# Kernel tuning notes

Measured on AMD Instinct MI355X. Metric: run time of the kernel, lower is better.

## Reference

```python
import jax, jax.numpy as jnp
import numpy as np

B, C, H, W = 2, 256, 64, 64
HEADS = 4
K = 64  # max attendable keys per query
GROUPS = 32
EPS = 1e-6


def group_norm(x, scale, bias):
    b, c, h, w = x.shape
    xg = x.reshape(b, GROUPS, c // GROUPS, h, w)
    mean = xg.mean(axis=(2, 3, 4), keepdims=True)
    var = xg.var(axis=(2, 3, 4), keepdims=True)
    xn = ((xg - mean) * jax.lax.rsqrt(var + EPS)).reshape(b, c, h, w)
    return xn * scale[None, :, None, None] + bias[None, :, None, None]


def conv1x1(x, w, b):
    return jnp.einsum('oc,bchw->bohw', w, x) + b[None, :, None, None]


def setup_inputs() -> dict:
    key = jax.random.key(0)
    ks = jax.random.split(key, 8)
    x = jax.random.normal(ks[0], (B, C, H, W), dtype=jnp.float32)
    valid_indices_mask = jax.random.randint(ks[1], (H * W, K), 0, 2, dtype=jnp.int32)
    attendable_indices = jax.random.randint(ks[2], (H * W, K), 0, H * W, dtype=jnp.int32)
    s = 0.02
    wq = jax.random.normal(ks[3], (C, C), dtype=jnp.float32) * s
    wk = jax.random.normal(ks[4], (C, C), dtype=jnp.float32) * s
    wv = jax.random.normal(ks[5], (C, C), dtype=jnp.float32) * s
    wo = jax.random.normal(ks[6], (C, C), dtype=jnp.float32) * s
    return {
        'x': x,
        'valid_indices_mask': valid_indices_mask,
        'attendable_indices': attendable_indices,
        'gn_scale': jnp.ones((C,), jnp.float32),
        'gn_bias': jnp.zeros((C,), jnp.float32),
        'wq': wq, 'bq': jnp.zeros((C,), jnp.float32),
        'wk': wk, 'bk': jnp.zeros((C,), jnp.float32),
        'wv': wv, 'bv': jnp.zeros((C,), jnp.float32),
        'wo': wo, 'bo': jnp.zeros((C,), jnp.float32),
    }


def reference(x, valid_indices_mask, attendable_indices, gn_scale, gn_bias,
              wq, bq, wk, bk, wv, bv, wo, bo):
    b, c, h, w = x.shape
    nq = h * w
    d = c // HEADS
    h_ = group_norm(x, gn_scale, gn_bias)
    q = conv1x1(h_, wq, bq).reshape(b, HEADS, d, nq)
    k = conv1x1(h_, wk, bk).reshape(b, HEADS, d, nq)
    v = conv1x1(h_, wv, bv).reshape(b, HEADS, d, nq)
    # gather per-query attendable keys/values: [b, heads, nq, K, d]
    kt = k.transpose(0, 1, 3, 2)  # [b, heads, nv, d]
    vt = v.transpose(0, 1, 3, 2)
    ak = kt[:, :, attendable_indices]  # [b, heads, nq, K, d]
    av = vt[:, :, attendable_indices]
    # beta = 1 (no 1/sqrt(d) scaling in the sparse path, per original code)
    logits = jnp.einsum('bhqkc,bhcq->bhqk', ak, q)
    neg = jnp.where(valid_indices_mask == 0, -jnp.inf, 0.0).astype(logits.dtype)
    logits = logits + neg[None, None, :, :]
    weights = jax.nn.softmax(logits, axis=-1)
    attn = jnp.einsum('bhqk,bhqkc->bhqc', weights, av)  # [b, heads, nq, d]
    attn = attn.transpose(0, 3, 1, 2).reshape(b, c, h, w)
    out = x + conv1x1(attn, wo, bo)
    return out
```

## Files before the change

kernel.cpp:

```cpp
#include <hip/hip_runtime.h>
#include <math.h>

typedef unsigned int uint;
typedef unsigned short ushort;
typedef __attribute__((ext_vector_type(8))) short bf16x8;
typedef __attribute__((ext_vector_type(4))) float f32x4;

#define LSTR 40

__device__ __forceinline__ float bf2f(ushort u) { return __uint_as_float(((uint)u) << 16); }
__device__ __forceinline__ ushort f2bf(float f) {
    uint u = __float_as_uint(f);
    return (ushort)((u + 0x7fffu + ((u >> 16) & 1u)) >> 16);
}

__global__ __launch_bounds__(256) void gn_part_k(const float* __restrict__ x,
                                                 float* __restrict__ stats) {
    const int bg = blockIdx.x >> 2, part = blockIdx.x & 3;
    const float4* base = (const float4*)(x + (size_t)bg * 32768 + part * 8192);
    float s = 0.f, ss = 0.f;
    for (int i = threadIdx.x; i < 2048; i += 256) {
        float4 v = base[i];
        s  += v.x + v.y + v.z + v.w;
        ss += v.x*v.x + v.y*v.y + v.z*v.z + v.w*v.w;
    }
    #pragma unroll
    for (int o = 32; o; o >>= 1) { s += __shfl_xor(s, o); ss += __shfl_xor(ss, o); }
    if ((threadIdx.x & 63) == 0) {
        atomicAdd(&stats[bg * 2],     s);
        atomicAdd(&stats[bg * 2 + 1], ss);
    }
}

__global__ __launch_bounds__(256) void gn_apply_t_k(const float* __restrict__ x,
        const float* __restrict__ stats, const float* __restrict__ sc,
        const float* __restrict__ bi, ushort* __restrict__ hT) {
    const int n0 = blockIdx.x * 64, c0 = blockIdx.y * 64, b = blockIdx.z;
    __shared__ ushort tile[64][65];
    const int t = threadIdx.x;
    #pragma unroll
    for (int it = 0; it < 4; ++it) {
        const int r = (t >> 4) + it * 16, col4 = t & 15;
        const int c = c0 + r, bg = b * 32 + (c >> 3);
        const float S = stats[bg * 2], SS = stats[bg * 2 + 1];
        const float mean = S * (1.f / 32768.f);
        const float var  = SS * (1.f / 32768.f) - mean * mean;
        const float a  = rsqrtf(var + 1e-6f) * sc[c];
        const float bb = bi[c] - mean * a;
        float4 v = *(const float4*)(x + ((size_t)(b * 256 + c)) * 4096 + n0 + col4 * 4);
        tile[r][col4*4 + 0] = f2bf(v.x * a + bb);
        tile[r][col4*4 + 1] = f2bf(v.y * a + bb);
        tile[r][col4*4 + 2] = f2bf(v.z * a + bb);
        tile[r][col4*4 + 3] = f2bf(v.w * a + bb);
    }
    __syncthreads();
    #pragma unroll
    for (int it = 0; it < 2; ++it) {
        const int nr = (t >> 3) + it * 32, c8 = t & 7;
        uint4 st;
        ushort e0 = tile[c8*8+0][nr], e1 = tile[c8*8+1][nr];
        ushort e2 = tile[c8*8+2][nr], e3 = tile[c8*8+3][nr];
        ushort e4 = tile[c8*8+4][nr], e5 = tile[c8*8+5][nr];
        ushort e6 = tile[c8*8+6][nr], e7 = tile[c8*8+7][nr];
        st.x = (uint)e0 | ((uint)e1 << 16);
        st.y = (uint)e2 | ((uint)e3 << 16);
        st.z = (uint)e4 | ((uint)e5 << 16);
        st.w = (uint)e6 | ((uint)e7 << 16);
        *(uint4*)(hT + ((size_t)b * 4096 + n0 + nr) * 256 + c0 + c8 * 8) = st;
    }
}

__global__ __launch_bounds__(256) void wprep_k(
        const float* __restrict__ wq, const float* __restrict__ wk,
        const float* __restrict__ wv, const float* __restrict__ wo,
        const float* __restrict__ bq, const float* __restrict__ bk,
        const float* __restrict__ bv,
        ushort* __restrict__ wqkv, ushort* __restrict__ wo_p,
        float* __restrict__ bqkv) {
    const int i = blockIdx.x * 256 + threadIdx.x;
    if (i < 196608) {
        const int o = i >> 8, k = i & 255;
        const float* W = (o < 256) ? wq : ((o < 512) ? wk : wv);
        wqkv[i] = f2bf(W[(o & 255) * 256 + k]);
    } else if (i < 262144) {
        const int j = i - 196608;
        const int o = j >> 8, kp = j & 255;
        const int h = kp >> 6, d = kp & 63;
        wo_p[j] = f2bf(wo[o * 256 + d * 4 + h]);
    } else if (i < 262912) {
        const int o = i - 262144;
        bqkv[o] = (o < 256) ? bq[o] : ((o < 512) ? bk[o - 256] : bv[o - 512]);
    }
}

__global__ __launch_bounds__(256) void qkv_gemm_k(
        const ushort* __restrict__ Wqkv, const float* __restrict__ bqkv,
        const ushort* __restrict__ hT, ushort* __restrict__ qkvb) {
    const int nt = blockIdx.x, mt = blockIdx.y, b = blockIdx.z;
    __shared__ ushort As[128 * LSTR];
    __shared__ ushort Bs[128 * LSTR];
    const int t = threadIdx.x;
    const int wave = t >> 6, ln = t & 63;
    const int wm = wave >> 1, wn = wave & 1;
    f32x4 acc[4][4] = {};
    const ushort* Ag = Wqkv + (size_t)(mt * 128) * 256;
    const ushort* Bg = hT + ((size_t)b * 4096 + nt * 128) * 256;
    const int srow = t >> 2, sc8 = (t & 3) * 8;
    const int fr = ln & 15, kA = (ln >> 4) * 8;

    for (int k0 = 0; k0 < 256; k0 += 32) {
        #pragma unroll
        for (int i = 0; i < 2; ++i) {
            const int row = srow + i * 64;
            *(uint4*)&As[row * LSTR + sc8] = *(const uint4*)&Ag[(size_t)row * 256 + k0 + sc8];
            *(uint4*)&Bs[row * LSTR + sc8] = *(const uint4*)&Bg[(size_t)row * 256 + k0 + sc8];
        }
        __syncthreads();
        bf16x8 af[4], bfr[4];
        #pragma unroll
        for (int m = 0; m < 4; ++m) af[m]  = *(bf16x8*)&As[(wm * 64 + m * 16 + fr) * LSTR + kA];
        #pragma unroll
        for (int n = 0; n < 4; ++n) bfr[n] = *(bf16x8*)&Bs[(wn * 64 + n * 16 + fr) * LSTR + kA];
        #pragma unroll
        for (int m = 0; m < 4; ++m)
            #pragma unroll
            for (int n = 0; n < 4; ++n)
                acc[m][n] = __builtin_amdgcn_mfma_f32_16x16x32_bf16(af[m], bfr[n], acc[m][n], 0, 0, 0);
        __syncthreads();
    }
    const int colb = nt * 128 + wn * 64 + fr;
    const int rowb = mt * 128 + wm * 64;
    #pragma unroll
    for (int m = 0; m < 4; ++m) {
        const int o0 = rowb + m * 16 + ((ln >> 4) << 2);
        const int proj = o0 >> 8;
        const int head = (o0 >> 6) & 3;
        const int d0 = o0 & 63;
        const float4 bi4 = *(const float4*)&bqkv[o0];
        ushort* obase = qkvb + ((size_t)proj * 8 + (b * 4 + head)) * (4096 * 64) + d0;
        #pragma unroll
        for (int n = 0; n < 4; ++n) {
            const int nn = colb + n * 16;
            f32x4 a = acc[m][n];
            uint2 st;
            st.x = (uint)f2bf(a[0] + bi4.x) | ((uint)f2bf(a[1] + bi4.y) << 16);
            st.y = (uint)f2bf(a[2] + bi4.z) | ((uint)f2bf(a[3] + bi4.w) << 16);
            *(uint2*)&obase[(size_t)nn * 64] = st;
        }
    }
}

__global__ __launch_bounds__(256) void attn_k(
        const ushort* __restrict__ qb, const ushort* __restrict__ kb,
        const ushort* __restrict__ vb, const int* __restrict__ aidx,
        const int* __restrict__ vmask, ushort* __restrict__ attnb) {
    const int bh = blockIdx.x & 7;
    const int q4 = blockIdx.x >> 3;
    const int wave = threadIdx.x >> 6, ln = threadIdx.x & 63;
    const int n = q4 * 4 + wave;
    const ushort* kbase = kb + (size_t)bh * (4096 * 64);
    const ushort* vbase = vb + (size_t)bh * (4096 * 64);
    __shared__ float q_lds[4][64];
    q_lds[wave][ln] = bf2f(qb[(size_t)bh * (4096 * 64) + (size_t)n * 64 + ln]);
    const int idx = aidx[n * 64 + ln];
    const int msk = vmask[n * 64 + ln];
    __syncthreads();

    float dot = 0.f;
    if (msk) {
        const uint4* krow = (const uint4*)(kbase + (size_t)idx * 64);
        const float* qv = q_lds[wave];
        #pragma unroll
        for (int c = 0; c < 8; ++c) {
            uint4 u = krow[c];
            dot += __uint_as_float(u.x << 16)         * qv[c*8+0];
            dot += __uint_as_float(u.x & 0xffff0000u) * qv[c*8+1];
            dot += __uint_as_float(u.y << 16)         * qv[c*8+2];
            dot += __uint_as_float(u.y & 0xffff0000u) * qv[c*8+3];
            dot += __uint_as_float(u.z << 16)         * qv[c*8+4];
            dot += __uint_as_float(u.z & 0xffff0000u) * qv[c*8+5];
            dot += __uint_as_float(u.w << 16)         * qv[c*8+6];
            dot += __uint_as_float(u.w & 0xffff0000u) * qv[c*8+7];
        }
    }
    float mx = msk ? dot : -1e30f;
    #pragma unroll
    for (int o = 32; o; o >>= 1) mx = fmaxf(mx, __shfl_xor(mx, o));
    float e = msk ? __expf(dot - mx) : 0.f;
    float s = e;
    #pragma unroll
    for (int o = 32; o; o >>= 1) s += __shfl_xor(s, o);
    const float wgt = e / s;

    float a0 = 0.f, a1 = 0.f, a2 = 0.f, a3 = 0.f;
    #pragma unroll
    for (int kk = 0; kk < 64; kk += 4) {
        const float w0 = __shfl(wgt, kk),     w1 = __shfl(wgt, kk + 1);
        const float w2 = __shfl(wgt, kk + 2), w3 = __shfl(wgt, kk + 3);
        const int i0 = __shfl(idx, kk),     i1 = __shfl(idx, kk + 1);
        const int i2 = __shfl(idx, kk + 2), i3 = __shfl(idx, kk + 3);
        a0 += w0 * bf2f(vbase[(size_t)i0 * 64 + ln]);
        a1 += w1 * bf2f(vbase[(size_t)i1 * 64 + ln]);
        a2 += w2 * bf2f(vbase[(size_t)i2 * 64 + ln]);
        a3 += w3 * bf2f(vbase[(size_t)i3 * 64 + ln]);
    }
    const int b = bh >> 2, h = bh & 3;
    attnb[((size_t)b * 4096 + n) * 256 + h * 64 + ln] = f2bf(a0 + a1 + a2 + a3);
}

__global__ __launch_bounds__(256) void out_gemm_k(
        const ushort* __restrict__ wo_p, const float* __restrict__ bo,
        const ushort* __restrict__ attnb, const float* __restrict__ x,
        float* __restrict__ outp) {
    const int nt = blockIdx.x, mt = blockIdx.y, b = blockIdx.z;
    __shared__ ushort As[128 * LSTR];
    __shared__ ushort Bs[128 * LSTR];
    const int t = threadIdx.x;
    const int wave = t >> 6, ln = t & 63;
    const int wm = wave >> 1, wn = wave & 1;
    f32x4 acc[4][4] = {};
    const ushort* Ag = wo_p + (size_t)(mt * 128) * 256;
    const ushort* Bg = attnb + ((size_t)b * 4096 + nt * 128) * 256;
    const int srow = t >> 2, sc8 = (t & 3) * 8;
    const int fr = ln & 15, kA = (ln >> 4) * 8;

    for (int k0 = 0; k0 < 256; k0 += 32) {
        #pragma unroll
        for (int i = 0; i < 2; ++i) {
            const int row = srow + i * 64;
            *(uint4*)&As[row * LSTR + sc8] = *(const uint4*)&Ag[(size_t)row * 256 + k0 + sc8];
            *(uint4*)&Bs[row * LSTR + sc8] = *(const uint4*)&Bg[(size_t)row * 256 + k0 + sc8];
        }
        __syncthreads();
        bf16x8 af[4], bfr[4];
        #pragma unroll
        for (int m = 0; m < 4; ++m) af[m]  = *(bf16x8*)&As[(wm * 64 + m * 16 + fr) * LSTR + kA];
        #pragma unroll
        for (int n = 0; n < 4; ++n) bfr[n] = *(bf16x8*)&Bs[(wn * 64 + n * 16 + fr) * LSTR + kA];
        #pragma unroll
        for (int m = 0; m < 4; ++m)
            #pragma unroll
            for (int n = 0; n < 4; ++n)
                acc[m][n] = __builtin_amdgcn_mfma_f32_16x16x32_bf16(af[m], bfr[n], acc[m][n], 0, 0, 0);
        __syncthreads();
    }
    const int colb = nt * 128 + wn * 64 + fr;
    const int rowb = mt * 128 + wm * 64;
    #pragma unroll
    for (int m = 0; m < 4; ++m) {
        const int o0 = rowb + m * 16 + ((ln >> 4) << 2);
        const float4 bi4 = *(const float4*)&bo[o0];
        const float* bip = (const float*)&bi4;
        #pragma unroll
        for (int n = 0; n < 4; ++n) {
            const int nn = colb + n * 16;
            #pragma unroll
            for (int r = 0; r < 4; ++r) {
                const size_t a = ((size_t)(b * 256 + o0 + r)) * 4096 + nn;
                outp[a] = acc[m][n][r] + bip[r] + x[a];
            }
        }
    }
}

extern "C" void kernel_launch(void* const* d_in, const int* in_sizes, int n_in,
                              void* d_out, int out_size, void* d_ws, size_t ws_size,
                              hipStream_t stream) {
    const float* x     = (const float*)d_in[0];
    const int*   vmask = (const int*)d_in[1];
    const int*   aidx  = (const int*)d_in[2];
    const float* gsc   = (const float*)d_in[3];
    const float* gbi   = (const float*)d_in[4];
    const float* wq    = (const float*)d_in[5];
    const float* bq    = (const float*)d_in[6];
    const float* wk    = (const float*)d_in[7];
    const float* bk    = (const float*)d_in[8];
    const float* wv    = (const float*)d_in[9];
    const float* bv    = (const float*)d_in[10];
    const float* wo    = (const float*)d_in[11];
    const float* bo    = (const float*)d_in[12];
    float* outp = (float*)d_out;

    char* w = (char*)d_ws;
    float*  stats = (float*)w;
    ushort* wqkv  = (ushort*)(w + 1024);
    ushort* wo_p  = (ushort*)(w + 1024 + 393216);
    float*  bqkv  = (float*)(w + 525312);
    ushort* hT    = (ushort*)(w + 528384);
    ushort* qkvb  = (ushort*)(w + 4722688);
    ushort* attnb = (ushort*)(w + 17305600);

    ushort* qbuf = qkvb;
    ushort* kbuf = qkvb + 2097152;
    ushort* vbuf = qkvb + 4194304;

    hipMemsetAsync(stats, 0, 512, stream);
    hipLaunchKernelGGL(gn_part_k,    dim3(256),        dim3(256), 0, stream, x, stats);
    hipLaunchKernelGGL(wprep_k,      dim3(1027),       dim3(256), 0, stream,
                       wq, wk, wv, wo, bq, bk, bv, wqkv, wo_p, bqkv);
    hipLaunchKernelGGL(gn_apply_t_k, dim3(64, 4, 2),   dim3(256), 0, stream,
                       x, stats, gsc, gbi, hT);
    hipLaunchKernelGGL(qkv_gemm_k,   dim3(32, 6, 2),   dim3(256), 0, stream,
                       wqkv, bqkv, hT, qkvb);
    hipLaunchKernelGGL(attn_k,       dim3(8192),       dim3(256), 0, stream,
                       qbuf, kbuf, vbuf, aidx, vmask, attnb);
    hipLaunchKernelGGL(out_gemm_k,   dim3(32, 2, 2),   dim3(256), 0, stream,
                       wo_p, bo, attnb, x, outp);
}
```

Measured before the change: 195.0 us.

## Shrink GEMM tiles, keep Q in fp32, and vectorize sparse attention gathers with readlane

The QKV and output GEMMs use smaller N (and M for output) tiles, giving more blocks and better occupancy on the many-CU GPU. Q is now stored in fp32 and broadcast with readlane instead of passing through LDS with a barrier. The V gather now has each lane load 4 contiguous bf16 values for one of four keys at once, followed by a cross-quarter shuffle reduction, so there are fewer load instructions. The K dot product now runs unconditionally with four accumulators. Costs are extra fp32 Q memory traffic, wasted loads for masked keys, and lower per-block tile reuse.

Measured after the change: 173.4 us. 1.12x faster.

```diff
diff --git a/kernel.cpp b/kernel.cpp
--- a/kernel.cpp
+++ b/kernel.cpp
@@ -12,6 +12,10 @@
 __device__ __forceinline__ ushort f2bf(float f) {
     uint u = __float_as_uint(f);
     return (ushort)((u + 0x7fffu + ((u >> 16) & 1u)) >> 16);
+}
+__device__ __forceinline__ int   RLI(int v, int l)   { return __builtin_amdgcn_readlane(v, l); }
+__device__ __forceinline__ float RLF(float v, int l) {
+    return __int_as_float(__builtin_amdgcn_readlane(__float_as_int(v), l));
 }
 
 __global__ __launch_bounds__(256) void gn_part_k(const float* __restrict__ x,
@@ -95,40 +99,38 @@
 
 __global__ __launch_bounds__(256) void qkv_gemm_k(
         const ushort* __restrict__ Wqkv, const float* __restrict__ bqkv,
-        const ushort* __restrict__ hT, ushort* __restrict__ qkvb) {
+        const ushort* __restrict__ hT, float* __restrict__ qf,
+        ushort* __restrict__ kvb) {
     const int nt = blockIdx.x, mt = blockIdx.y, b = blockIdx.z;
     __shared__ ushort As[128 * LSTR];
-    __shared__ ushort Bs[128 * LSTR];
+    __shared__ ushort Bs[64 * LSTR];
     const int t = threadIdx.x;
     const int wave = t >> 6, ln = t & 63;
     const int wm = wave >> 1, wn = wave & 1;
-    f32x4 acc[4][4] = {};
+    f32x4 acc[4][2] = {};
     const ushort* Ag = Wqkv + (size_t)(mt * 128) * 256;
-    const ushort* Bg = hT + ((size_t)b * 4096 + nt * 128) * 256;
+    const ushort* Bg = hT + ((size_t)b * 4096 + nt * 64) * 256;
     const int srow = t >> 2, sc8 = (t & 3) * 8;
     const int fr = ln & 15, kA = (ln >> 4) * 8;
 
     for (int k0 = 0; k0 < 256; k0 += 32) {
-        #pragma unroll
-        for (int i = 0; i < 2; ++i) {
-            const int row = srow + i * 64;
-            *(uint4*)&As[row * LSTR + sc8] = *(const uint4*)&Ag[(size_t)row * 256 + k0 + sc8];
-            *(uint4*)&Bs[row * LSTR + sc8] = *(const uint4*)&Bg[(size_t)row * 256 + k0 + sc8];
-        }
+        *(uint4*)&As[srow * LSTR + sc8]        = *(const uint4*)&Ag[(size_t)srow * 256 + k0 + sc8];
+        *(uint4*)&As[(srow + 64) * LSTR + sc8] = *(const uint4*)&Ag[(size_t)(srow + 64) * 256 + k0 + sc8];
+        *(uint4*)&Bs[srow * LSTR + sc8]        = *(const uint4*)&Bg[(size_t)srow * 256 + k0 + sc8];
         __syncthreads();
-        bf16x8 af[4], bfr[4];
+        bf16x8 af[4], bfr[2];
         #pragma unroll
         for (int m = 0; m < 4; ++m) af[m]  = *(bf16x8*)&As[(wm * 64 + m * 16 + fr) * LSTR + kA];
         #pragma unroll
-        for (int n = 0; n < 4; ++n) bfr[n] = *(bf16x8*)&Bs[(wn * 64 + n * 16 + fr) * LSTR + kA];
+        for (int n = 0; n < 2; ++n) bfr[n] = *(bf16x8*)&Bs[(wn * 32 + n * 16 + fr) * LSTR + kA];
         #pragma unroll
         for (int m = 0; m < 4; ++m)
             #pragma unroll
-            for (int n = 0; n < 4; ++n)
+            for (int n = 0; n < 2; ++n)
                 acc[m][n] = __builtin_amdgcn_mfma_f32_16x16x32_bf16(af[m], bfr[n], acc[m][n], 0, 0, 0);
         __syncthreads();
     }
-    const int colb = nt * 128 + wn * 64 + fr;
+    const int colb = nt * 64 + wn * 32 + fr;
     const int rowb = mt * 128 + wm * 64;
     #pragma unroll
     for (int m = 0; m < 4; ++m) {
@@ -137,21 +139,32 @@
         const int head = (o0 >> 6) & 3;
         const int d0 = o0 & 63;
         const float4 bi4 = *(const float4*)&bqkv[o0];
-        ushort* obase = qkvb + ((size_t)proj * 8 + (b * 4 + head)) * (4096 * 64) + d0;
-        #pragma unroll
-        for (int n = 0; n < 4; ++n) {
-            const int nn = colb + n * 16;
-            f32x4 a = acc[m][n];
-            uint2 st;
-            st.x = (uint)f2bf(a[0] + bi4.x) | ((uint)f2bf(a[1] + bi4.y) << 16);
-            st.y = (uint)f2bf(a[2] + bi4.z) | ((uint)f2bf(a[3] + bi4.w) << 16);
-            *(uint2*)&obase[(size_t)nn * 64] = st;
+        if (proj == 0) {
+            float* obase = qf + ((size_t)(b * 4 + head) * 4096) * 64 + d0;
+            #pragma unroll
+            for (int n = 0; n < 2; ++n) {
+                const int nn = colb + n * 16;
+                f32x4 a = acc[m][n];
+                float4 st = { a[0] + bi4.x, a[1] + bi4.y, a[2] + bi4.z, a[3] + bi4.w };
+                *(float4*)&obase[(size_t)nn * 64] = st;
+            }
+        } else {
+            ushort* obase = kvb + ((size_t)(proj - 1) * 8 + (b * 4 + head)) * (4096 * 64) + d0;
+            #pragma unroll
+            for (int n = 0; n < 2; ++n) {
+                const int nn = colb + n * 16;
+                f32x4 a = acc[m][n];
+                uint2 st;
+                st.x = (uint)f2bf(a[0] + bi4.x) | ((uint)f2bf(a[1] + bi4.y) << 16);
+                st.y = (uint)f2bf(a[2] + bi4.z) | ((uint)f2bf(a[3] + bi4.w) << 16);
+                *(uint2*)&obase[(size_t)nn * 64] = st;
+            }
         }
     }
 }
 
 __global__ __launch_bounds__(256) void attn_k(
-        const ushort* __restrict__ qb, const ushort* __restrict__ kb,
+        const float* __restrict__ qf, const ushort* __restrict__ kb,
         const ushort* __restrict__ vb, const int* __restrict__ aidx,
         const int* __restrict__ vmask, ushort* __restrict__ attnb) {
     const int bh = blockIdx.x & 7;
@@ -160,52 +173,66 @@
     const int n = q4 * 4 + wave;
     const ushort* kbase = kb + (size_t)bh * (4096 * 64);
     const ushort* vbase = vb + (size_t)bh * (4096 * 64);
-    __shared__ float q_lds[4][64];
-    q_lds[wave][ln] = bf2f(qb[(size_t)bh * (4096 * 64) + (size_t)n * 64 + ln]);
+    const float qreg = qf[((size_t)bh * 4096 + n) * 64 + ln];
     const int idx = aidx[n * 64 + ln];
     const int msk = vmask[n * 64 + ln];
-    __syncthreads();
-
-    float dot = 0.f;
-    if (msk) {
+
+    float d0 = 0.f, d1 = 0.f, d2 = 0.f, d3 = 0.f;
+    {
         const uint4* krow = (const uint4*)(kbase + (size_t)idx * 64);
-        const float* qv = q_lds[wave];
         #pragma unroll
         for (int c = 0; c < 8; ++c) {
             uint4 u = krow[c];
-            dot += __uint_as_float(u.x << 16)         * qv[c*8+0];
-            dot += __uint_as_float(u.x & 0xffff0000u) * qv[c*8+1];
-            dot += __uint_as_float(u.y << 16)         * qv[c*8+2];
-            dot += __uint_as_float(u.y & 0xffff0000u) * qv[c*8+3];
-            dot += __uint_as_float(u.z << 16)         * qv[c*8+4];
-            dot += __uint_as_float(u.z & 0xffff0000u) * qv[c*8+5];
-            dot += __uint_as_float(u.w << 16)         * qv[c*8+6];
-            dot += __uint_as_float(u.w & 0xffff0000u) * qv[c*8+7];
+            d0 += __uint_as_float(u.x << 16)         * RLF(qreg, c*8 + 0);
+            d1 += __uint_as_float(u.x & 0xffff0000u) * RLF(qreg, c*8 + 1);
+            d2 += __uint_as_float(u.y << 16)         * RLF(qreg, c*8 + 2);
+            d3 += __uint_as_float(u.y & 0xffff0000u) * RLF(qreg, c*8 + 3);
+            d0 += __uint_as_float(u.z << 16)         * RLF(qreg, c*8 + 4);
+            d1 += __uint_as_float(u.z & 0xffff0000u) * RLF(qreg, c*8 + 5);
+            d2 += __uint_as_float(u.w << 16)         * RLF(qreg, c*8 + 6);
+            d3 += __uint_as_float(u.w & 0xffff0000u) * RLF(qreg, c*8 + 7);
         }
     }
+    const float dot = (d0 + d1) + (d2 + d3);
     float mx = msk ? dot : -1e30f;
     #pragma unroll
     for (int o = 32; o; o >>= 1) mx = fmaxf(mx, __shfl_xor(mx, o));
-    float e = msk ? __expf(dot - mx) : 0.f;
+    const float e = msk ? __expf(dot - mx) : 0.f;
     float s = e;
     #pragma unroll
     for (int o = 32; o; o >>= 1) s += __shfl_xor(s, o);
     const float wgt = e / s;
 
+    const int p = ln >> 4, d4 = ln & 15;
+    const bool c1 = (p == 1), c2 = (p == 2), c3 = (p == 3);
     float a0 = 0.f, a1 = 0.f, a2 = 0.f, a3 = 0.f;
-    #pragma unroll
-    for (int kk = 0; kk < 64; kk += 4) {
-        const float w0 = __shfl(wgt, kk),     w1 = __shfl(wgt, kk + 1);
-        const float w2 = __shfl(wgt, kk + 2), w3 = __shfl(wgt, kk + 3);
-        const int i0 = __shfl(idx, kk),     i1 = __shfl(idx, kk + 1);
-        const int i2 = __shfl(idx, kk + 2), i3 = __shfl(idx, kk + 3);
-        a0 += w0 * bf2f(vbase[(size_t)i0 * 64 + ln]);
-        a1 += w1 * bf2f(vbase[(size_t)i1 * 64 + ln]);
-        a2 += w2 * bf2f(vbase[(size_t)i2 * 64 + ln]);
-        a3 += w3 * bf2f(vbase[(size_t)i3 * 64 + ln]);
-    }
-    const int b = bh >> 2, h = bh & 3;
-    attnb[((size_t)b * 4096 + n) * 256 + h * 64 + ln] = f2bf(a0 + a1 + a2 + a3);
+    const ushort* vb2 = vbase + d4 * 4;
+    #pragma unroll
+    for (int k = 0; k < 64; k += 4) {
+        const int   i0 = RLI(idx, k),     i1 = RLI(idx, k + 1);
+        const int   i2 = RLI(idx, k + 2), i3 = RLI(idx, k + 3);
+        const float w0 = RLF(wgt, k),     w1 = RLF(wgt, k + 1);
+        const float w2 = RLF(wgt, k + 2), w3 = RLF(wgt, k + 3);
+        int   si = c1 ? i1 : i0; si = c2 ? i2 : si; si = c3 ? i3 : si;
+        float sw = c1 ? w1 : w0; sw = c2 ? w2 : sw; sw = c3 ? w3 : sw;
+        const uint2 u = *(const uint2*)(vb2 + (size_t)si * 64);
+        a0 += sw * __uint_as_float(u.x << 16);
+        a1 += sw * __uint_as_float(u.x & 0xffff0000u);
+        a2 += sw * __uint_as_float(u.y << 16);
+        a3 += sw * __uint_as_float(u.y & 0xffff0000u);
+    }
+    #pragma unroll
+    for (int o = 16; o <= 32; o <<= 1) {
+        a0 += __shfl_xor(a0, o); a1 += __shfl_xor(a1, o);
+        a2 += __shfl_xor(a2, o); a3 += __shfl_xor(a3, o);
+    }
+    if (p == 0) {
+        const int b = bh >> 2, h = bh & 3;
+        uint2 st;
+        st.x = (uint)f2bf(a0) | ((uint)f2bf(a1) << 16);
+        st.y = (uint)f2bf(a2) | ((uint)f2bf(a3) << 16);
+        *(uint2*)(attnb + ((size_t)b * 4096 + n) * 256 + h * 64 + d4 * 4) = st;
+    }
 }
 
 __global__ __launch_bounds__(256) void out_gemm_k(
@@ -213,46 +240,42 @@
         const ushort* __restrict__ attnb, const float* __restrict__ x,
         float* __restrict__ outp) {
     const int nt = blockIdx.x, mt = blockIdx.y, b = blockIdx.z;
-    __shared__ ushort As[128 * LSTR];
-    __shared__ ushort Bs[128 * LSTR];
+    __shared__ ushort As[64 * LSTR];
+    __shared__ ushort Bs[64 * LSTR];
     const int t = threadIdx.x;
     const int wave = t >> 6, ln = t & 63;
     const int wm = wave >> 1, wn = wave & 1;
-    f32x4 acc[4][4] = {};
-    const ushort* Ag = wo_p + (size_t)(mt * 128) * 256;
-    const ushort* Bg = attnb + ((size_t)b * 4096 + nt * 128) * 256;
+    f32x4 acc[2][2] = {};
+    const ushort* Ag = wo_p + (size_t)(mt * 64) * 256;
+    const ushort* Bg = attnb + ((size_t)b * 4096 + nt * 64) * 256;
     const int srow = t >> 2, sc8 = (t & 3) * 8;
     const int fr = ln & 15, kA = (ln >> 4) * 8;
 
     for (int k0 = 0; k0 < 256; k0 += 32) {
-        #pragma unroll
-        for (int i = 0; i < 2; ++i) {
-            const int row = srow + i * 64;
-            *(uint4*)&As[row * LSTR + sc8] = *(const uint4*)&Ag[(size_t)row * 256 + k0 + sc8];
-            *(uint4*)&Bs[row * LSTR + sc8] = *(const uint4*)&Bg[(size_t)row * 256 + k0 + sc8];
-        }
+        *(uint4*)&As[srow * LSTR + sc8] = *(const uint4*)&Ag[(size_t)srow * 256 + k0 + sc8];
+        *(uint4*)&Bs[srow * LSTR + sc8] = *(const uint4*)&Bg[(size_t)srow * 256 + k0 + sc8];
         __syncthreads();
-        bf16x8 af[4], bfr[4];
-        #pragma unroll
-        for (int m = 0; m < 4; ++m) af[m]  = *(bf16x8*)&As[(wm * 64 + m * 16 + fr) * LSTR + kA];
-        #pragma unroll
-        for (int n = 0; n < 4; ++n) bfr[n] = *(bf16x8*)&Bs[(wn * 64 + n * 16 + fr) * LSTR + kA];
-        #pragma unroll
-        for (int m = 0; m < 4; ++m)
-            #pragma unroll
-            for (int n = 0; n < 4; ++n)
+        bf16x8 af[2], bfr[2];
+        #pragma unroll
+        for (int m = 0; m < 2; ++m) af[m]  = *(bf16x8*)&As[(wm * 32 + m * 16 + fr) * LSTR + kA];
+        #pragma unroll
+        for (int n = 0; n < 2; ++n) bfr[n] = *(bf16x8*)&Bs[(wn * 32 + n * 16 + fr) * LSTR + kA];
+        #pragma unroll
+        for (int m = 0; m < 2; ++m)
+            #pragma unroll
+            for (int n = 0; n < 2; ++n)
                 acc[m][n] = __builtin_amdgcn_mfma_f32_16x16x32_bf16(af[m], bfr[n], acc[m][n], 0, 0, 0);
         __syncthreads();
     }
-    const int colb = nt * 128 + wn * 64 + fr;
-    const int rowb = mt * 128 + wm * 64;
-    #pragma unroll
-    for (int m = 0; m < 4; ++m) {
+    const int colb = nt * 64 + wn * 32 + fr;
+    const int rowb = mt * 64 + wm * 32;
+    #pragma unroll
+    for (int m = 0; m < 2; ++m) {
         const int o0 = rowb + m * 16 + ((ln >> 4) << 2);
         const float4 bi4 = *(const float4*)&bo[o0];
         const float* bip = (const float*)&bi4;
         #pragma unroll
-        for (int n = 0; n < 4; ++n) {
+        for (int n = 0; n < 2; ++n) {
             const int nn = colb + n * 16;
             #pragma unroll
             for (int r = 0; r < 4; ++r) {
@@ -284,15 +307,15 @@
     char* w = (char*)d_ws;
     float*  stats = (float*)w;
     ushort* wqkv  = (ushort*)(w + 1024);
-    ushort* wo_p  = (ushort*)(w + 1024 + 393216);
+    ushort* wo_p  = (ushort*)(w + 394240);
     float*  bqkv  = (float*)(w + 525312);
     ushort* hT    = (ushort*)(w + 528384);
-    ushort* qkvb  = (ushort*)(w + 4722688);
-    ushort* attnb = (ushort*)(w + 17305600);
-
-    ushort* qbuf = qkvb;
-    ushort* kbuf = qkvb + 2097152;
-    ushort* vbuf = qkvb + 4194304;
+    float*  qf    = (float*)(w + 4722688);
+    ushort* kvb   = (ushort*)(w + 13111296);
+    ushort* attnb = (ushort*)(w + 21499904);
+
+    ushort* kbuf = kvb;
+    ushort* vbuf = kvb + 2097152;
 
     hipMemsetAsync(stats, 0, 512, stream);
     hipLaunchKernelGGL(gn_part_k,    dim3(256),        dim3(256), 0, stream, x, stats);
@@ -300,10 +323,10 @@
                        wq, wk, wv, wo, bq, bk, bv, wqkv, wo_p, bqkv);
     hipLaunchKernelGGL(gn_apply_t_k, dim3(64, 4, 2),   dim3(256), 0, stream,
                        x, stats, gsc, gbi, hT);
-    hipLaunchKernelGGL(qkv_gemm_k,   dim3(32, 6, 2),   dim3(256), 0, stream,
-                       wqkv, bqkv, hT, qkvb);
+    hipLaunchKernelGGL(qkv_gemm_k,   dim3(64, 6, 2),   dim3(256), 0, stream,
+                       wqkv, bqkv, hT, qf, kvb);
     hipLaunchKernelGGL(attn_k,       dim3(8192),       dim3(256), 0, stream,
-                       qbuf, kbuf, vbuf, aidx, vmask, attnb);
-    hipLaunchKernelGGL(out_gemm_k,   dim3(32, 2, 2),   dim3(256), 0, stream,
+                       qf, kbuf, vbuf, aidx, vmask, attnb);
+    hipLaunchKernelGGL(out_gemm_k,   dim3(64, 4, 2),   dim3(256), 0, stream,
                        wo_p, bo, attnb, x, outp);
 }
```
